# Optimization experiments

Hardware: AMD Instinct MI355X
Metric: run time of the kernel (lower is better)

Reference implementation:

```python
import jax, jax.numpy as jnp
import numpy as np

N, L, E, H = 4, 2048, 1024, 16
DK = E // H  # 64

def setup_inputs() -> dict:
    key = jax.random.key(0)
    ks = jax.random.split(key, 5)
    scale = 0.02
    return {
        "x": jax.random.normal(ks[0], (N, L, E), dtype=jnp.float32),
        "Wq": jax.random.normal(ks[1], (E, E), dtype=jnp.float32) * scale,
        "Wk": jax.random.normal(ks[2], (E, E), dtype=jnp.float32) * scale,
        "Wv": jax.random.normal(ks[3], (E, E), dtype=jnp.float32) * scale,
        "Wo": jax.random.normal(ks[4], (E, E), dtype=jnp.float32) * scale,
    }

def reference(x, Wq, Wk, Wv, Wo):
    n, l, _ = x.shape
    # nn.Linear(bias=False): y = x @ W.T
    q = x @ Wq.T  # (n, l, H*DK)
    k = x @ Wk.T
    v = x @ Wv.T
    # Faithful to torch .view: plain reshape (NOT transpose-based head split)
    q = q.reshape(n, H, l, DK)
    k = k.reshape(n, H, l, DK)
    v = v.reshape(n, H, l, DK)
    scores = jnp.einsum('nhqd,nhkd->nhqk', q, k) / jnp.sqrt(jnp.float32(DK))
    attn = jax.nn.softmax(scores, axis=-1)
    out = jnp.einsum('nhqk,nhkd->nhqd', attn, v).reshape(n, l, H * DK)
    return out @ Wo.T
```

## Files before the change

kernel.cpp:

```cpp
#include <hip/hip_runtime.h>


#define DEVI __device__ __forceinline__

typedef _Float16 half8 __attribute__((ext_vector_type(8)));
typedef _Float16 half4v __attribute__((ext_vector_type(4)));
typedef float f32x4 __attribute__((ext_vector_type(4)));

DEVI void gload_lds16(const void* g, void* l) {
    __builtin_amdgcn_global_load_lds(
        (const __attribute__((address_space(1))) void*)g,
        (__attribute__((address_space(3))) void*)l,
        16, 0, 0);
}

DEVI f32x4 zero4() { f32x4 z = {0.f, 0.f, 0.f, 0.f}; return z; }

#if __has_builtin(__builtin_amdgcn_exp2f)
DEVI float fast_exp2(float x) { return __builtin_amdgcn_exp2f(x); }
#else
DEVI float fast_exp2(float x) { return exp2f(x); }
#endif

DEVI half8 lds_read8_swz(const _Float16* base, int row, int colbyte) {
    const char* p = (const char*)base;
    const int off = (row * 128 + colbyte) ^ ((row & 7) << 4);
    return *(const half8*)(p + off);
}

__global__ __launch_bounds__(256) void f2h_kernel(const float* __restrict__ s,
                                                  _Float16* __restrict__ d) {
    const size_t i = (size_t)blockIdx.x * 256 + threadIdx.x;
    const float4 v = ((const float4*)s)[i];
    half4v h;
    h[0] = (_Float16)v.x; h[1] = (_Float16)v.y;
    h[2] = (_Float16)v.z; h[3] = (_Float16)v.w;
    ((half4v*)d)[i] = h;
}

template<int MODE>
__global__ __launch_bounds__(256) void gemm_k(const _Float16* __restrict__ A,
                                              const _Float16* __restrict__ B,
                                              void* __restrict__ Cout,
                                              float qscale) {
    constexpr int NBLK = (MODE == 0) ? 24 : 8;
    constexpr int CPX  = (MODE == 0) ? 192 : 64;
    alignas(16) __shared__ _Float16 As[128 * 64];
    alignas(16) __shared__ _Float16 Bs[128 * 64];
    const int t = threadIdx.x;
    const int lane = t & 63;
    const int w = t >> 6;
    const int wr = (w >> 1) * 64;
    const int wc = (w & 1) * 64;
    const int nid = (blockIdx.x & 7) * CPX + (blockIdx.x >> 3);
    const int bn = (nid % NBLK) * 128;
    const int bm = (nid / NBLK) * 128;
    const int r16 = lane & 15;
    const int q4 = lane >> 4;
    const int sr = t >> 3;
    const int sc8 = (t & 7) * 8;

    f32x4 acc[4][4];
    #pragma unroll
    for (int mi = 0; mi < 4; ++mi)
        #pragma unroll
        for (int ni = 0; ni < 4; ++ni)
            acc[mi][ni] = zero4();

    for (int kt = 0; kt < 1024; kt += 64) {
        #pragma unroll
        for (int i = 0; i < 4; ++i) {
            gload_lds16(A + (size_t)(bm + i * 32 + sr) * 1024 + kt + sc8, &As[i * 2048 + t * 8]);
            gload_lds16(B + (size_t)(bn + i * 32 + sr) * 1024 + kt + sc8, &Bs[i * 2048 + t * 8]);
        }
        __syncthreads();
        #pragma unroll
        for (int kk = 0; kk < 2; ++kk) {
            half8 a[4], b[4];
            #pragma unroll
            for (int mi = 0; mi < 4; ++mi)
                a[mi] = *(const half8*)&As[(wr + mi * 16 + r16) * 64 + kk * 32 + q4 * 8];
            #pragma unroll
            for (int ni = 0; ni < 4; ++ni)
                b[ni] = *(const half8*)&Bs[(wc + ni * 16 + r16) * 64 + kk * 32 + q4 * 8];
            #pragma unroll
            for (int mi = 0; mi < 4; ++mi)
                #pragma unroll
                for (int ni = 0; ni < 4; ++ni)
                    acc[mi][ni] = __builtin_amdgcn_mfma_f32_16x16x32_f16(a[mi], b[ni], acc[mi][ni], 0, 0, 0);
        }
        __syncthreads();
    }
    if (MODE == 0) {
        const int which = bn >> 10;
        const int cb = bn & 1023;
        const float alpha = (which == 0) ? qscale : 1.0f;
        _Float16* C = (_Float16*)Cout + (size_t)which * 8388608;
        #pragma unroll
        for (int mi = 0; mi < 4; ++mi) {
            const int row = bm + wr + mi * 16 + q4 * 4;
            #pragma unroll
            for (int ni = 0; ni < 4; ++ni) {
                const int col = cb + wc + ni * 16 + r16;
                #pragma unroll
                for (int i = 0; i < 4; ++i)
                    C[(size_t)(row + i) * 1024 + col] = (_Float16)(acc[mi][ni][i] * alpha);
            }
        }
    } else {
        float* C = (float*)Cout;
        #pragma unroll
        for (int mi = 0; mi < 4; ++mi) {
            const int row = bm + wr + mi * 16 + q4 * 4;
            #pragma unroll
            for (int ni = 0; ni < 4; ++ni) {
                const int col = bn + wc + ni * 16 + r16;
                #pragma unroll
                for (int i = 0; i < 4; ++i)
                    C[(size_t)(row + i) * 1024 + col] = acc[mi][ni][i];
            }
        }
    }
}

__global__ __launch_bounds__(256) void transpose_v(const _Float16* __restrict__ V,
                                                   _Float16* __restrict__ Vt) {
    __shared__ unsigned short lds[64 * 65];
    const int t = threadIdx.x;
    const int kt = blockIdx.x;
    const size_t hb = (size_t)blockIdx.y * 131072;
    const int r = t >> 2;
    const int c0 = (t & 3) * 16;
    const unsigned short* Vi = (const unsigned short*)V;
    #pragma unroll
    for (int j = 0; j < 2; ++j) {
        union { uint4 u; unsigned short s[8]; } tmp;
        tmp.u = *(const uint4*)&Vi[hb + (size_t)(kt * 64 + r) * 64 + c0 + j * 8];
        #pragma unroll
        for (int e = 0; e < 8; ++e)
            lds[r * 65 + c0 + j * 8 + e] = tmp.s[e];
    }
    __syncthreads();
    unsigned short* Vo = (unsigned short*)Vt;
    #pragma unroll
    for (int j = 0; j < 16; ++j) {
        const int idx = j * 256 + t;
        const int d = idx >> 6;
        const int c = idx & 63;
        Vo[hb + (size_t)d * 2048 + kt * 64 + c] = lds[c * 65 + d];
    }
}

__global__ __launch_bounds__(256) void attn_kernel(const _Float16* __restrict__ Q,
                                                   const _Float16* __restrict__ K,
                                                   const _Float16* __restrict__ Vt,
                                                   _Float16* __restrict__ O) {
    alignas(16) __shared__ _Float16 Ks[2][64 * 64];
    alignas(16) __shared__ _Float16 Vs[2][64 * 64];
    alignas(16) __shared__ _Float16 Ps[4][32 * 64];
    const int t = threadIdx.x;
    const int lane = t & 63;
    const int w = t >> 6;
    const int nid = (blockIdx.x & 7) * 128 + (blockIdx.x >> 3);
    const size_t hb = (size_t)(nid >> 4) * 131072;
    const int qt = nid & 15;
    const int r16 = lane & 15;
    const int q4 = lane >> 4;
    const int sr = t >> 3;
    const int sc = t & 7;

    half8 aq[2][2];
    const int q0 = qt * 128 + w * 32;
    #pragma unroll
    for (int mi = 0; mi < 2; ++mi)
        #pragma unroll
        for (int kk = 0; kk < 2; ++kk)
            aq[mi][kk] = *(const half8*)&Q[hb + (size_t)(q0 + mi * 16 + r16) * 64 + kk * 32 + q4 * 8];

    f32x4 o[2][4];
    float lsum[2][4];
    #pragma unroll
    for (int mi = 0; mi < 2; ++mi)
        #pragma unroll
        for (int i = 0; i < 4; ++i) lsum[mi][i] = 0.f;
    #pragma unroll
    for (int mi = 0; mi < 2; ++mi)
        #pragma unroll
        for (int ni = 0; ni < 4; ++ni)
            o[mi][ni] = zero4();

    _Float16* Pw = Ps[w];

    const int R0 = sr, R1 = 32 + sr;
    const int scs0 = (sc ^ (R0 & 7)) * 8;
    const int scs1 = (sc ^ (R1 & 7)) * 8;

    {
        gload_lds16(&K[hb + (size_t)R0 * 64 + scs0],        &Ks[0][t * 8]);
        gload_lds16(&K[hb + (size_t)R1 * 64 + scs1],        &Ks[0][2048 + t * 8]);
        gload_lds16(&Vt[hb + (size_t)R0 * 2048 + scs0],     &Vs[0][t * 8]);
        gload_lds16(&Vt[hb + (size_t)R1 * 2048 + scs1],     &Vs[0][2048 + t * 8]);
    }
    __syncthreads();

    int pb = 0;
    for (int kt = 0; kt < 32; ++kt) {
        if (kt + 1 < 32) {
            const size_t kb = hb + (size_t)(kt + 1) * 64 * 64;
            gload_lds16(&K[kb + (size_t)R0 * 64 + scs0],                 &Ks[pb ^ 1][t * 8]);
            gload_lds16(&K[kb + (size_t)R1 * 64 + scs1],                 &Ks[pb ^ 1][2048 + t * 8]);
            gload_lds16(&Vt[hb + (size_t)R0 * 2048 + (kt + 1) * 64 + scs0], &Vs[pb ^ 1][t * 8]);
            gload_lds16(&Vt[hb + (size_t)R1 * 2048 + (kt + 1) * 64 + scs1], &Vs[pb ^ 1][2048 + t * 8]);
        }

        f32x4 s[2][4];
        #pragma unroll
        for (int mi = 0; mi < 2; ++mi)
            #pragma unroll
            for (int ni = 0; ni < 4; ++ni)
                s[mi][ni] = zero4();
        __builtin_amdgcn_s_setprio(1);
        #pragma unroll
        for (int kk = 0; kk < 2; ++kk) {
            half8 bk[4];
            #pragma unroll
            for (int ni = 0; ni < 4; ++ni)
                bk[ni] = lds_read8_swz(Ks[pb], ni * 16 + r16, (kk * 32 + q4 * 8) * 2);
            #pragma unroll
            for (int mi = 0; mi < 2; ++mi)
                #pragma unroll
                for (int ni = 0; ni < 4; ++ni)
                    s[mi][ni] = __builtin_amdgcn_mfma_f32_16x16x32_f16(aq[mi][kk], bk[ni], s[mi][ni], 0, 0, 0);
        }
        __builtin_amdgcn_s_setprio(0);

        #pragma unroll
        for (int mi = 0; mi < 2; ++mi)
            #pragma unroll
            for (int i = 0; i < 4; ++i) {
                const int pr = mi * 16 + q4 * 4 + i;
                float rs = 0.f;
                #pragma unroll
                for (int ni = 0; ni < 4; ++ni) {
                    const float p = fast_exp2(s[mi][ni][i]);
                    rs += p;
                    const int off = ((pr * 128 + (ni * 16 + r16) * 2) ^ ((pr & 7) << 4));
                    *(_Float16*)((char*)Pw + off) = (_Float16)p;
                }
                lsum[mi][i] += rs;
            }

        __builtin_amdgcn_s_setprio(1);
        #pragma unroll
        for (int kk = 0; kk < 2; ++kk) {
            half8 ap[2], bv[4];
            #pragma unroll
            for (int mi = 0; mi < 2; ++mi)
                ap[mi] = lds_read8_swz(Pw, mi * 16 + r16, (kk * 32 + q4 * 8) * 2);
            #pragma unroll
            for (int ni = 0; ni < 4; ++ni)
                bv[ni] = lds_read8_swz(Vs[pb], ni * 16 + r16, (kk * 32 + q4 * 8) * 2);
            #pragma unroll
            for (int mi = 0; mi < 2; ++mi)
                #pragma unroll
                for (int ni = 0; ni < 4; ++ni)
                    o[mi][ni] = __builtin_amdgcn_mfma_f32_16x16x32_f16(ap[mi], bv[ni], o[mi][ni], 0, 0, 0);
        }
        __builtin_amdgcn_s_setprio(0);

        __syncthreads();
        pb ^= 1;
    }

    #pragma unroll
    for (int mi = 0; mi < 2; ++mi)
        #pragma unroll
        for (int i = 0; i < 4; ++i) {
            float l = lsum[mi][i];
            l += __shfl_xor(l, 1);
            l += __shfl_xor(l, 2);
            l += __shfl_xor(l, 4);
            l += __shfl_xor(l, 8);
            const float inv = 1.f / l;
            const int row = q0 + mi * 16 + q4 * 4 + i;
            #pragma unroll
            for (int ni = 0; ni < 4; ++ni)
                O[hb + (size_t)row * 64 + ni * 16 + r16] = (_Float16)(o[mi][ni][i] * inv);
        }
}

extern "C" void kernel_launch(void* const* d_in, const int* in_sizes, int n_in,
                              void* d_out, int out_size, void* d_ws, size_t ws_size,
                              hipStream_t stream) {
    const float* x  = (const float*)d_in[0];
    const float* Wq = (const float*)d_in[1];
    const float* Wk = (const float*)d_in[2];
    const float* Wv = (const float*)d_in[3];
    const float* Wo = (const float*)d_in[4];

    const size_t XSZ = (size_t)8192 * 1024;
    const size_t WSZ = (size_t)1024 * 1024;

    _Float16* ws  = (_Float16*)d_ws;
    _Float16* xh  = ws;
    _Float16* wqh = ws + XSZ;
    _Float16* wkh = wqh + WSZ;
    _Float16* wvh = wkh + WSZ;
    _Float16* woh = wvh + WSZ;
    _Float16* qh  = woh + WSZ;
    _Float16* kh  = qh + XSZ;
    _Float16* vh  = kh + XSZ;
    _Float16* aoh = vh + XSZ;
    _Float16* vth = xh;

    f2h_kernel<<<XSZ / 4 / 256, 256, 0, stream>>>(x,  xh);
    f2h_kernel<<<WSZ / 4 / 256, 256, 0, stream>>>(Wq, wqh);
    f2h_kernel<<<WSZ / 4 / 256, 256, 0, stream>>>(Wk, wkh);
    f2h_kernel<<<WSZ / 4 / 256, 256, 0, stream>>>(Wv, wvh);
    f2h_kernel<<<WSZ / 4 / 256, 256, 0, stream>>>(Wo, woh);

    const float qscale = 0.125f * 1.44269504088896340736f;

    gemm_k<0><<<1536, 256, 0, stream>>>(xh, wqh, (void*)qh, qscale);

    transpose_v<<<dim3(32, 64), 256, 0, stream>>>(vh, vth);

    attn_kernel<<<1024, 256, 0, stream>>>(qh, kh, vth, aoh);

    gemm_k<1><<<512, 256, 0, stream>>>(aoh, woh, d_out, 1.0f);
    (void)in_sizes; (void)n_in; (void)out_size; (void)ws_size;
}
```

Measured before the change: 309.5 us.

## Compute transposed scores to keep P in registers, dropping LDS round-trip

Result: no change. 305.9 us (-1.2%).

```diff
diff --git a/kernel.cpp b/kernel.cpp
--- a/kernel.cpp
+++ b/kernel.cpp
@@ -4,7 +4,7 @@
 #define DEVI __device__ __forceinline__
 
 typedef _Float16 half8 __attribute__((ext_vector_type(8)));
-typedef _Float16 half4v __attribute__((ext_vector_type(4)));
+typedef _Float16 half4 __attribute__((ext_vector_type(4)));
 typedef float f32x4 __attribute__((ext_vector_type(4)));
 
 DEVI void gload_lds16(const void* g, void* l) {
@@ -22,20 +22,37 @@
 DEVI float fast_exp2(float x) { return exp2f(x); }
 #endif
 
+#if __has_builtin(__builtin_amdgcn_mfma_f32_16x16x16f16)
+DEVI f32x4 mfma16(half4 a, half4 b, f32x4 c) {
+    return __builtin_amdgcn_mfma_f32_16x16x16f16(a, b, c, 0, 0, 0);
+}
+#else
+DEVI f32x4 mfma16(half4 a, half4 b, f32x4 c) {
+    asm volatile("v_mfma_f32_16x16x16_f16 %0, %1, %2, %0"
+                 : "+v"(c) : "v"(a), "v"(b));
+    return c;
+}
+#endif
+
 DEVI half8 lds_read8_swz(const _Float16* base, int row, int colbyte) {
     const char* p = (const char*)base;
     const int off = (row * 128 + colbyte) ^ ((row & 7) << 4);
     return *(const half8*)(p + off);
 }
+DEVI half4 lds_read4_swz(const _Float16* base, int row, int colbyte) {
+    const char* p = (const char*)base;
+    const int off = (row * 128 + colbyte) ^ ((row & 7) << 4);
+    return *(const half4*)(p + off);
+}
 
 __global__ __launch_bounds__(256) void f2h_kernel(const float* __restrict__ s,
                                                   _Float16* __restrict__ d) {
     const size_t i = (size_t)blockIdx.x * 256 + threadIdx.x;
     const float4 v = ((const float4*)s)[i];
-    half4v h;
+    half4 h;
     h[0] = (_Float16)v.x; h[1] = (_Float16)v.y;
     h[2] = (_Float16)v.z; h[3] = (_Float16)v.w;
-    ((half4v*)d)[i] = h;
+    ((half4*)d)[i] = h;
 }
 
 template<int MODE>
@@ -157,7 +174,6 @@
                                                    _Float16* __restrict__ O) {
     alignas(16) __shared__ _Float16 Ks[2][64 * 64];
     alignas(16) __shared__ _Float16 Vs[2][64 * 64];
-    alignas(16) __shared__ _Float16 Ps[4][32 * 64];
     const int t = threadIdx.x;
     const int lane = t & 63;
     const int w = t >> 6;
@@ -177,19 +193,13 @@
         for (int kk = 0; kk < 2; ++kk)
             aq[mi][kk] = *(const half8*)&Q[hb + (size_t)(q0 + mi * 16 + r16) * 64 + kk * 32 + q4 * 8];
 
-    f32x4 o[2][4];
-    float lsum[2][4];
-    #pragma unroll
-    for (int mi = 0; mi < 2; ++mi)
-        #pragma unroll
-        for (int i = 0; i < 4; ++i) lsum[mi][i] = 0.f;
-    #pragma unroll
-    for (int mi = 0; mi < 2; ++mi)
-        #pragma unroll
-        for (int ni = 0; ni < 4; ++ni)
-            o[mi][ni] = zero4();
-
-    _Float16* Pw = Ps[w];
+    f32x4 o[4][2];
+    float lsum[2] = {0.f, 0.f};
+    #pragma unroll
+    for (int ni = 0; ni < 4; ++ni)
+        #pragma unroll
+        for (int mi = 0; mi < 2; ++mi)
+            o[ni][mi] = zero4();
 
     const int R0 = sr, R1 = 32 + sr;
     const int scs0 = (sc ^ (R0 & 7)) * 8;
@@ -213,80 +223,79 @@
             gload_lds16(&Vt[hb + (size_t)R1 * 2048 + (kt + 1) * 64 + scs1], &Vs[pb ^ 1][2048 + t * 8]);
         }
 
-        f32x4 s[2][4];
-        #pragma unroll
-        for (int mi = 0; mi < 2; ++mi)
-            #pragma unroll
-            for (int ni = 0; ni < 4; ++ni)
-                s[mi][ni] = zero4();
+        f32x4 sT[4][2];
+        #pragma unroll
+        for (int ki = 0; ki < 4; ++ki)
+            #pragma unroll
+            for (int mi = 0; mi < 2; ++mi)
+                sT[ki][mi] = zero4();
         __builtin_amdgcn_s_setprio(1);
         #pragma unroll
         for (int kk = 0; kk < 2; ++kk) {
-            half8 bk[4];
-            #pragma unroll
-            for (int ni = 0; ni < 4; ++ni)
-                bk[ni] = lds_read8_swz(Ks[pb], ni * 16 + r16, (kk * 32 + q4 * 8) * 2);
-            #pragma unroll
-            for (int mi = 0; mi < 2; ++mi)
-                #pragma unroll
-                for (int ni = 0; ni < 4; ++ni)
-                    s[mi][ni] = __builtin_amdgcn_mfma_f32_16x16x32_f16(aq[mi][kk], bk[ni], s[mi][ni], 0, 0, 0);
+            half8 ak[4];
+            #pragma unroll
+            for (int ki = 0; ki < 4; ++ki)
+                ak[ki] = lds_read8_swz(Ks[pb], ki * 16 + r16, (kk * 32 + q4 * 8) * 2);
+            #pragma unroll
+            for (int ki = 0; ki < 4; ++ki)
+                #pragma unroll
+                for (int mi = 0; mi < 2; ++mi)
+                    sT[ki][mi] = __builtin_amdgcn_mfma_f32_16x16x32_f16(ak[ki], aq[mi][kk], sT[ki][mi], 0, 0, 0);
         }
         __builtin_amdgcn_s_setprio(0);
 
-        #pragma unroll
-        for (int mi = 0; mi < 2; ++mi)
-            #pragma unroll
-            for (int i = 0; i < 4; ++i) {
-                const int pr = mi * 16 + q4 * 4 + i;
-                float rs = 0.f;
-                #pragma unroll
-                for (int ni = 0; ni < 4; ++ni) {
-                    const float p = fast_exp2(s[mi][ni][i]);
-                    rs += p;
-                    const int off = ((pr * 128 + (ni * 16 + r16) * 2) ^ ((pr & 7) << 4));
-                    *(_Float16*)((char*)Pw + off) = (_Float16)p;
-                }
-                lsum[mi][i] += rs;
+        half4 pT[4][2];
+        #pragma unroll
+        for (int ki = 0; ki < 4; ++ki)
+            #pragma unroll
+            for (int mi = 0; mi < 2; ++mi) {
+                const float p0 = fast_exp2(sT[ki][mi][0]);
+                const float p1 = fast_exp2(sT[ki][mi][1]);
+                const float p2 = fast_exp2(sT[ki][mi][2]);
+                const float p3 = fast_exp2(sT[ki][mi][3]);
+                lsum[mi] += (p0 + p1) + (p2 + p3);
+                half4 pv;
+                pv[0] = (_Float16)p0; pv[1] = (_Float16)p1;
+                pv[2] = (_Float16)p2; pv[3] = (_Float16)p3;
+                pT[ki][mi] = pv;
             }
 
         __builtin_amdgcn_s_setprio(1);
         #pragma unroll
-        for (int kk = 0; kk < 2; ++kk) {
-            half8 ap[2], bv[4];
-            #pragma unroll
-            for (int mi = 0; mi < 2; ++mi)
-                ap[mi] = lds_read8_swz(Pw, mi * 16 + r16, (kk * 32 + q4 * 8) * 2);
-            #pragma unroll
-            for (int ni = 0; ni < 4; ++ni)
-                bv[ni] = lds_read8_swz(Vs[pb], ni * 16 + r16, (kk * 32 + q4 * 8) * 2);
-            #pragma unroll
-            for (int mi = 0; mi < 2; ++mi)
-                #pragma unroll
-                for (int ni = 0; ni < 4; ++ni)
-                    o[mi][ni] = __builtin_amdgcn_mfma_f32_16x16x32_f16(ap[mi], bv[ni], o[mi][ni], 0, 0, 0);
-        }
+        for (int ki = 0; ki < 4; ++ki)
+            #pragma unroll
+            for (int ni = 0; ni < 4; ++ni) {
+                const half4 av = lds_read4_swz(Vs[pb], ni * 16 + r16, ki * 32 + q4 * 8);
+                #pragma unroll
+                for (int mi = 0; mi < 2; ++mi)
+                    o[ni][mi] = mfma16(av, pT[ki][mi], o[ni][mi]);
+            }
         __builtin_amdgcn_s_setprio(0);
 
         __syncthreads();
         pb ^= 1;
     }
 
-    #pragma unroll
-    for (int mi = 0; mi < 2; ++mi)
-        #pragma unroll
-        for (int i = 0; i < 4; ++i) {
-            float l = lsum[mi][i];
-            l += __shfl_xor(l, 1);
-            l += __shfl_xor(l, 2);
-            l += __shfl_xor(l, 4);
-            l += __shfl_xor(l, 8);
-            const float inv = 1.f / l;
-            const int row = q0 + mi * 16 + q4 * 4 + i;
-            #pragma unroll
-            for (int ni = 0; ni < 4; ++ni)
-                O[hb + (size_t)row * 64 + ni * 16 + r16] = (_Float16)(o[mi][ni][i] * inv);
-        }
+    float inv[2];
+    #pragma unroll
+    for (int mi = 0; mi < 2; ++mi) {
+        float l = lsum[mi];
+        l += __shfl_xor(l, 16);
+        l += __shfl_xor(l, 32);
+        inv[mi] = 1.f / l;
+    }
+    #pragma unroll
+    for (int mi = 0; mi < 2; ++mi) {
+        const int q = q0 + mi * 16 + r16;
+        #pragma unroll
+        for (int ni = 0; ni < 4; ++ni) {
+            half4 ov;
+            #pragma unroll
+            for (int i = 0; i < 4; ++i)
+                ov[i] = (_Float16)(o[ni][mi][i] * inv[mi]);
+            *(half4*)&O[hb + (size_t)q * 64 + ni * 16 + q4 * 4] = ov;
+        }
+    }
 }
 
 extern "C" void kernel_launch(void* const* d_in, const int* in_sizes, int n_in,
```
